# Performance work log

Measured on AMD Instinct MI355X. Metric: run time of the kernel, lower is better.

Reference implementation:

```python
import jax, jax.numpy as jnp
import numpy as np

N = 100000   # nodes
S = 2        # layout samples per graph
G = 8        # graphs in batch
E = 400000   # directed edges
MID = 256    # mid_ch
L = 4        # n_layer
CLN = 2      # concat_last_n
IN_CH = 53 + 32 + 6 * 23 + 6 * 3 + 6 * 4  # 265


def setup_inputs() -> dict:
    key = jax.random.key(0)
    ks = jax.random.split(key, 16)
    f = lambda k, sh: jax.random.normal(k, sh, dtype=jnp.float32)
    return {
        "x_feat": f(ks[0], (N, 53)),
        "dim_feat": f(ks[1], (N, 6, 23)),
        "layout_feat": f(ks[2], (N, S, 6, 4)),
        "tile_feat": f(ks[3], (G, S, 6, 3)),
        "opcode_embed": f(ks[4], (121, 32)) * 0.02,
        "preW": f(ks[5], (IN_CH, MID)) * 0.05,
        "preb": jnp.zeros((MID,), jnp.float32),
        "convWl": f(ks[6], (L, MID, MID // 2)) * 0.05,
        "convWr": f(ks[7], (L, MID, MID // 2)) * 0.05,
        "convb": jnp.zeros((L, MID // 2), jnp.float32),
        "revWl": f(ks[8], (L, MID, MID // 2)) * 0.05,
        "revWr": f(ks[9], (L, MID, MID // 2)) * 0.05,
        "revb": jnp.zeros((L, MID // 2), jnp.float32),
        "headW": f(ks[10], (MID * CLN, 1)) * 0.05,
        "headb": jnp.zeros((1,), jnp.float32),
        "node_opcode": jax.random.randint(ks[11], (N,), 0, 121),
        "batch": jnp.sort(jax.random.randint(ks[12], (N,), 0, G)),
        "edge_index": jax.random.randint(ks[13], (2, E), 0, N),
    }


def _sage(x, src, tgt, inv_deg, Wl, Wr, b):
    # PyG SAGEConv: out = lin_l(mean_{j->i} x_j) + lin_r(x_i) + bias
    # x: [S, N, C]; gather messages from src, scatter-add into tgt.
    agg = jnp.zeros_like(x).at[:, tgt].add(x[:, src])
    agg = agg * inv_deg[None, :, None]
    return (jnp.einsum('snc,co->sno', agg, Wl)
            + jnp.einsum('snc,co->sno', x, Wr) + b)


def reference(x_feat, dim_feat, layout_feat, tile_feat, opcode_embed,
              preW, preb, convWl, convWr, convb, revWl, revWr, revb,
              headW, headb, node_opcode, batch, edge_index):
    op = opcode_embed[node_opcode]                       # [N, 32]
    base = jnp.concatenate([x_feat, op, dim_feat.reshape(N, -1)], axis=-1)
    x = jnp.concatenate([
        jnp.broadcast_to(base[None], (S,) + base.shape),          # [S,N,223]
        layout_feat.transpose(1, 0, 2, 3).reshape(S, N, -1),       # [S,N,24]
        tile_feat[batch].transpose(1, 0, 2, 3).reshape(S, N, -1),  # [S,N,18]
    ], axis=-1)                                                    # [S,N,265]
    x = jax.nn.relu(x @ preW + preb)                               # [S,N,MID]

    src, tgt = edge_index[0], edge_index[1]
    one = jnp.ones((E,), x.dtype)
    inv_fwd = 1.0 / jnp.maximum(jnp.zeros((N,), x.dtype).at[tgt].add(one), 1.0)
    inv_rev = 1.0 / jnp.maximum(jnp.zeros((N,), x.dtype).at[src].add(one), 1.0)

    xs = []
    for i in range(L):
        x = jnp.concatenate([
            _sage(x, src, tgt, inv_fwd, convWl[i], convWr[i], convb[i]),
            _sage(x, tgt, src, inv_rev, revWl[i], revWr[i], revb[i]),
        ], axis=-1)
        x = jax.nn.relu(x)
        if i >= L - CLN:
            xs.append(x)
    x = jnp.concatenate(xs, axis=-1)                     # [S, N, MID*CLN]

    pooled = jnp.zeros((S, G, x.shape[-1]), x.dtype).at[:, batch].add(x)
    out = pooled @ headW + headb                         # [S, G, 1]
    return out.transpose(1, 0, 2)                        # [G, S, 1]
```

## Files before the change

### kernel.cpp

```cpp
#include <hip/hip_runtime.h>
#include <hip/hip_bf16.h>

#define N_NODES 100000
#define S_SAMP 2
#define G_GRAPH 8
#define E_EDGES 400000
#define NLAYER 4
#define IN_CH 265
#define KPRE 384
#define MT128 ((N_NODES + 127) / 128)
#define NPAD (MT128 * 128)
#define NG128 ((MT128 + 7) / 8)
#define NB1 ((N_NODES + 1023) / 1024)

typedef unsigned short u16;
typedef unsigned int u32;
typedef short bf16x8 __attribute__((ext_vector_type(8)));
typedef float f32x4 __attribute__((ext_vector_type(4)));

__device__ __forceinline__ float b2f(u16 u) {
    union { u32 i; float f; } x; x.i = ((u32)u) << 16; return x.f;
}
__device__ __forceinline__ u16 f2b(float f) {
    __hip_bfloat16 h = __float2bfloat16(f);
    return *reinterpret_cast<u16*>(&h);
}

__device__ __forceinline__ void gl_lds16(const u16* g, u16* l) {
    __builtin_amdgcn_global_load_lds(
        (const __attribute__((address_space(1))) void*)g,
        (__attribute__((address_space(3))) void*)l, 16, 0, 0);
}

__global__ __launch_bounds__(256) void build_s_k(const float* __restrict__ xf,
                                                 const float* __restrict__ dimf,
                                                 const float* __restrict__ layf,
                                                 const float* __restrict__ tilef,
                                                 const float* __restrict__ opemb,
                                                 const int* __restrict__ opcode,
                                                 const int* __restrict__ batch,
                                                 int s, u16* __restrict__ xin) {
    int item = blockIdx.x * blockDim.x + threadIdx.x;
    int n = item / 67;
    if (n >= N_NODES) return;
    int base = (item - n * 67) * 4;
    int opc = opcode[n];
    int g = batch[n];
    ushort4 o;
    u16* op = &o.x;
    #pragma unroll
    for (int u = 0; u < 4; u++) {
        int c = base + u;
        float v = 0.0f;
        if (c < 53)       v = xf[(size_t)n * 53 + c];
        else if (c < 85)  v = opemb[opc * 32 + (c - 53)];
        else if (c < 223) v = dimf[(size_t)n * 138 + (c - 85)];
        else if (c < 247) v = layf[((size_t)n * 2 + s) * 24 + (c - 223)];
        else if (c < 265) v = tilef[((size_t)g * 2 + s) * 18 + (c - 247)];
        op[u] = f2b(v);
    }
    *(ushort4*)(xin + (size_t)n * KPRE + base) = o;
}

__global__ void pack_w_k(const float* __restrict__ cWl, const float* __restrict__ rWl,
                         const float* __restrict__ cWr, const float* __restrict__ rWr,
                         const float* __restrict__ cb,  const float* __restrict__ rb,
                         u16* __restrict__ Wt, float* __restrict__ bcat) {
    int idx = blockIdx.x * blockDim.x + threadIdx.x;
    if (idx < NLAYER * 512 * 256) {
        int l = idx >> 17;
        int r = idx & 131071;
        int j = r >> 8;
        int k = r & 255;
        int jj = j & 255;
        int half = j >> 8;
        int sub = jj >> 7;
        int col = jj & 127;
        const float* src = half ? (sub ? rWl : cWl) : (sub ? rWr : cWr);
        Wt[idx] = f2b(src[((size_t)l * 256 + k) * 128 + col]);
    }
    if (idx < NLAYER * 512) {
        int l = idx >> 9;
        int j = idx & 511;
        float v = 0.0f;
        if (j < 256) v = (j < 128) ? cb[l * 128 + j] : rb[l * 128 + (j - 128)];
        bcat[idx] = v;
    }
}

__global__ void pack_pre_k(const float* __restrict__ preW, u16* __restrict__ preWt) {
    int idx = blockIdx.x * blockDim.x + threadIdx.x;
    if (idx >= 256 * KPRE) return;
    int j = idx / KPRE;
    int k = idx - j * KPRE;
    preWt[idx] = (k < IN_CH) ? f2b(preW[(size_t)k * 256 + j]) : (u16)0;
}

__global__ void deg_k(const int* __restrict__ ei, int* __restrict__ degF,
                      int* __restrict__ degR) {
    int e = blockIdx.x * blockDim.x + threadIdx.x;
    if (e < E_EDGES) {
        atomicAdd(&degF[ei[E_EDGES + e]], 1);
        atomicAdd(&degR[ei[e]], 1);
    }
}

__global__ __launch_bounds__(1024) void scan1_k(const int* __restrict__ degF,
                                                const int* __restrict__ degR,
                                                int* __restrict__ rpF,
                                                int* __restrict__ rpR,
                                                int* __restrict__ bsum) {
    const int* deg = blockIdx.y ? degR : degF;
    int* rp = blockIdx.y ? rpR : rpF;
    __shared__ int buf[1024];
    int i = blockIdx.x * 1024 + threadIdx.x;
    int v = (i < N_NODES) ? deg[i] : 0;
    buf[threadIdx.x] = v;
    __syncthreads();
    for (int off = 1; off < 1024; off <<= 1) {
        int t = (threadIdx.x >= off) ? buf[threadIdx.x - off] : 0;
        __syncthreads();
        buf[threadIdx.x] += t;
        __syncthreads();
    }
    if (i < N_NODES) rp[i] = buf[threadIdx.x] - v;
    if (threadIdx.x == 1023) bsum[blockIdx.y * NB1 + blockIdx.x] = buf[1023];
}

__global__ __launch_bounds__(256) void scan2_k(int* __restrict__ bsum,
                                               int* __restrict__ rpF,
                                               int* __restrict__ rpR) {
    __shared__ int buf[2][128];
    int half = threadIdx.x >> 7;
    int t = threadIdx.x & 127;
    int v = (t < NB1) ? bsum[half * NB1 + t] : 0;
    buf[half][t] = v;
    __syncthreads();
    for (int off = 1; off < 128; off <<= 1) {
        int x = (t >= off) ? buf[half][t - off] : 0;
        __syncthreads();
        buf[half][t] += x;
        __syncthreads();
    }
    if (t < NB1) bsum[half * NB1 + t] = buf[half][t] - v;
    if (t == NB1) (half ? rpR : rpF)[N_NODES] = buf[half][NB1 - 1];
}

__global__ void scan3_k(const int* __restrict__ bsum, int* __restrict__ rpF,
                        int* __restrict__ rpR) {
    int* rp = blockIdx.y ? rpR : rpF;
    int i = blockIdx.x * 1024 + threadIdx.x;
    if (i < N_NODES) rp[i] += bsum[blockIdx.y * NB1 + blockIdx.x];
}

__global__ void inv_cursor_k(const int* __restrict__ degF, const int* __restrict__ degR,
                             const int* __restrict__ rpF, const int* __restrict__ rpR,
                             float* __restrict__ invF, float* __restrict__ invR,
                             int* __restrict__ curF, int* __restrict__ curR) {
    int i = blockIdx.x * blockDim.x + threadIdx.x;
    if (i < N_NODES) {
        invF[i] = 1.0f / fmaxf((float)degF[i], 1.0f);
        invR[i] = 1.0f / fmaxf((float)degR[i], 1.0f);
        curF[i] = rpF[i];
        curR[i] = rpR[i];
    }
}

__global__ void fill_k(const int* __restrict__ ei, int* __restrict__ curF,
                       int* __restrict__ curR, int* __restrict__ colF,
                       int* __restrict__ colR) {
    int e = blockIdx.x * blockDim.x + threadIdx.x;
    if (e < E_EDGES) {
        int s = ei[e], t = ei[E_EDGES + e];
        colF[atomicAdd(&curF[t], 1)] = s;
        colR[atomicAdd(&curR[s], 1)] = t;
    }
}

template <bool RELU_OUT, int NCHUNK, int COLT>
__global__ __launch_bounds__(256) void mmB_k(const u16* __restrict__ A,
                                             const u16* __restrict__ Bt,
                                             const float* __restrict__ bias,
                                             u16* __restrict__ C0,
                                             u16* __restrict__ C1,
                                             int M) {
    __shared__ u16 As[128 * 128];
    __shared__ u16 Bs[64 * 128];
    constexpr int K = NCHUNK * 128;

    int bid = blockIdx.x;
    int x = bid & 7;
    int q = bid >> 3;
    int c = q % COLT;
    int g = q / COLT;
    int rowTile = g * 8 + x;
    if (rowTile >= MT128) return;
    int rowBase = rowTile * 128;
    int colBase = c * 64;

    int tid = threadIdx.x;
    int wv = tid >> 6;
    int lane = tid & 63;
    int quad = lane >> 4;
    int l16 = lane & 15;
    int rsub = lane >> 4;
    int sl = lane & 15;

    f32x4 acc[2][4] = {};

    for (int ci = 0; ci < NCHUNK; ci++) {
        int k0 = ci * 128;
        #pragma unroll
        for (int i = 0; i < 8; i++) {
            int r = wv * 32 + 4 * i + rsub;
            int ch = sl ^ (r & 15);
            gl_lds16(A + (size_t)(rowBase + r) * K + k0 + ch * 8,
                     As + (wv * 32 + 4 * i) * 128);
        }
        #pragma unroll
        for (int i = 0; i < 4; i++) {
            int r = wv * 16 + 4 * i + rsub;
            int ch = sl ^ (r & 15);
            gl_lds16(Bt + (size_t)(colBase + r) * K + k0 + ch * 8,
                     Bs + (wv * 16 + 4 * i) * 128);
        }
        __syncthreads();
        #pragma unroll
        for (int ks = 0; ks < 4; ks++) {
            int ca = ks * 4 + quad;
            bf16x8 af[2];
            #pragma unroll
            for (int rf = 0; rf < 2; rf++) {
                int ra = wv * 32 + rf * 16 + l16;
                af[rf] = *(const bf16x8*)(As + ra * 128 + (ca ^ (ra & 15)) * 8);
            }
            #pragma unroll
            for (int cf = 0; cf < 4; cf++) {
                int rb = cf * 16 + l16;
                bf16x8 bf = *(const bf16x8*)(Bs + rb * 128 + (ca ^ (rb & 15)) * 8);
                acc[0][cf] = __builtin_amdgcn_mfma_f32_16x16x32_bf16(af[0], bf, acc[0][cf], 0, 0, 0);
                acc[1][cf] = __builtin_amdgcn_mfma_f32_16x16x32_bf16(af[1], bf, acc[1][cf], 0, 0, 0);
            }
        }
        if (ci + 1 < NCHUNK) __syncthreads();
    }

    u16* dst = (colBase < 256) ? C0 : C1;
    int cb = colBase & 255;
    #pragma unroll
    for (int rf = 0; rf < 2; rf++) {
        #pragma unroll
        for (int cf = 0; cf < 4; cf++) {
            int col = cb + cf * 16 + l16;
            float bv = bias[colBase + cf * 16 + l16];
            #pragma unroll
            for (int r = 0; r < 4; r++) {
                int row = rowBase + wv * 32 + rf * 16 + quad * 4 + r;
                if (row < M) {
                    float v = acc[rf][cf][r] + bv;
                    if (RELU_OUT) v = fmaxf(v, 0.0f);
                    dst[(size_t)row * 256 + col] = f2b(v);
                }
            }
        }
    }
}

template <bool DOT>
__global__ __launch_bounds__(256) void agg_k(const int* __restrict__ rpF,
                                             const int* __restrict__ colF,
                                             const int* __restrict__ rpR,
                                             const int* __restrict__ colR,
                                             const float* __restrict__ invF,
                                             const float* __restrict__ invR,
                                             const u16* __restrict__ H,
                                             u16* __restrict__ Xn,
                                             const float* __restrict__ w,
                                             float* __restrict__ dotbuf) {
    int n = (blockIdx.x * blockDim.x + threadIdx.x) >> 6;
    if (n >= N_NODES) return;
    int lane = threadIdx.x & 63;
    int half = lane >> 5;
    int l32 = lane & 31;
    const int* rp  = half ? rpR : rpF;
    const int* col = half ? colR : colF;
    float inv = half ? invR[n] : invF[n];
    const u16* Hb = H + half * 128 + 4 * l32;

    float a0 = 0, a1 = 0, a2 = 0, a3 = 0;
    int b = rp[n], e = rp[n + 1];
    int j = b;
    for (; j + 7 < e; j += 8) {
        int c0 = col[j],     c1 = col[j + 1], c2 = col[j + 2], c3 = col[j + 3];
        int c4 = col[j + 4], c5 = col[j + 5], c6 = col[j + 6], c7 = col[j + 7];
        ushort4 h0 = *(const ushort4*)(Hb + (size_t)c0 * 256);
        ushort4 h1 = *(const ushort4*)(Hb + (size_t)c1 * 256);
        ushort4 h2 = *(const ushort4*)(Hb + (size_t)c2 * 256);
        ushort4 h3 = *(const ushort4*)(Hb + (size_t)c3 * 256);
        ushort4 h4 = *(const ushort4*)(Hb + (size_t)c4 * 256);
        ushort4 h5 = *(const ushort4*)(Hb + (size_t)c5 * 256);
        ushort4 h6 = *(const ushort4*)(Hb + (size_t)c6 * 256);
        ushort4 h7 = *(const ushort4*)(Hb + (size_t)c7 * 256);
        a0 += b2f(h0.x) + b2f(h1.x) + b2f(h2.x) + b2f(h3.x)
            + b2f(h4.x) + b2f(h5.x) + b2f(h6.x) + b2f(h7.x);
        a1 += b2f(h0.y) + b2f(h1.y) + b2f(h2.y) + b2f(h3.y)
            + b2f(h4.y) + b2f(h5.y) + b2f(h6.y) + b2f(h7.y);
        a2 += b2f(h0.z) + b2f(h1.z) + b2f(h2.z) + b2f(h3.z)
            + b2f(h4.z) + b2f(h5.z) + b2f(h6.z) + b2f(h7.z);
        a3 += b2f(h0.w) + b2f(h1.w) + b2f(h2.w) + b2f(h3.w)
            + b2f(h4.w) + b2f(h5.w) + b2f(h6.w) + b2f(h7.w);
    }
    for (; j + 3 < e; j += 4) {
        int c0 = col[j], c1 = col[j + 1], c2 = col[j + 2], c3 = col[j + 3];
        ushort4 h0 = *(const ushort4*)(Hb + (size_t)c0 * 256);
        ushort4 h1 = *(const ushort4*)(Hb + (size_t)c1 * 256);
        ushort4 h2 = *(const ushort4*)(Hb + (size_t)c2 * 256);
        ushort4 h3 = *(const ushort4*)(Hb + (size_t)c3 * 256);
        a0 += b2f(h0.x) + b2f(h1.x) + b2f(h2.x) + b2f(h3.x);
        a1 += b2f(h0.y) + b2f(h1.y) + b2f(h2.y) + b2f(h3.y);
        a2 += b2f(h0.z) + b2f(h1.z) + b2f(h2.z) + b2f(h3.z);
        a3 += b2f(h0.w) + b2f(h1.w) + b2f(h2.w) + b2f(h3.w);
    }
    for (; j < e; j++) {
        int c = col[j];
        ushort4 h = *(const ushort4*)(Hb + (size_t)c * 256);
        a0 += b2f(h.x); a1 += b2f(h.y); a2 += b2f(h.z); a3 += b2f(h.w);
    }
    u16* xp = Xn + (size_t)n * 256 + 4 * lane;
    ushort4 xv = *(const ushort4*)xp;
    float v0 = fmaxf(b2f(xv.x) + a0 * inv, 0.0f);
    float v1 = fmaxf(b2f(xv.y) + a1 * inv, 0.0f);
    float v2 = fmaxf(b2f(xv.z) + a2 * inv, 0.0f);
    float v3 = fmaxf(b2f(xv.w) + a3 * inv, 0.0f);
    ushort4 o;
    o.x = f2b(v0); o.y = f2b(v1); o.z = f2b(v2); o.w = f2b(v3);
    *(ushort4*)xp = o;
    if (DOT) {
        float4 wv4 = *(const float4*)(w + 4 * lane);
        float d = v0 * wv4.x + v1 * wv4.y + v2 * wv4.z + v3 * wv4.w;
        #pragma unroll
        for (int off = 32; off > 0; off >>= 1) d += __shfl_down(d, off);
        if (lane == 0) dotbuf[n] = d;
    }
}

__global__ void out_init_k(float* __restrict__ out, const float* __restrict__ headb) {
    int i = threadIdx.x;
    if (i < G_GRAPH * S_SAMP) out[i] = headb[0];
}

__global__ __launch_bounds__(256) void reduce_k(const float* __restrict__ dotbuf,
                                                const int* __restrict__ batch,
                                                float* __restrict__ out, int s) {
    __shared__ float part[G_GRAPH];
    if (threadIdx.x < G_GRAPH) part[threadIdx.x] = 0.0f;
    __syncthreads();
    for (int i = blockIdx.x * 256 + threadIdx.x; i < N_NODES; i += gridDim.x * 256)
        atomicAdd(&part[batch[i]], dotbuf[i]);
    __syncthreads();
    if (threadIdx.x < G_GRAPH)
        atomicAdd(&out[threadIdx.x * S_SAMP + s], part[threadIdx.x]);
}

extern "C" void kernel_launch(void* const* d_in, const int* in_sizes, int n_in,
                              void* d_out, int out_size, void* d_ws, size_t ws_size,
                              hipStream_t stream) {
    const float* x_feat      = (const float*)d_in[0];
    const float* dim_feat    = (const float*)d_in[1];
    const float* layout_feat = (const float*)d_in[2];
    const float* tile_feat   = (const float*)d_in[3];
    const float* opemb       = (const float*)d_in[4];
    const float* preW        = (const float*)d_in[5];
    const float* preb        = (const float*)d_in[6];
    const float* convWl      = (const float*)d_in[7];
    const float* convWr      = (const float*)d_in[8];
    const float* convb       = (const float*)d_in[9];
    const float* revWl       = (const float*)d_in[10];
    const float* revWr       = (const float*)d_in[11];
    const float* revb        = (const float*)d_in[12];
    const float* headW       = (const float*)d_in[13];
    const float* headb       = (const float*)d_in[14];
    const int*   node_opcode = (const int*)d_in[15];
    const int*   batch       = (const int*)d_in[16];
    const int*   edge_index  = (const int*)d_in[17];
    float* out = (float*)d_out;

    char* ws = (char*)d_ws;
    size_t off = 0;
    auto alloc = [&](size_t nbytes) {
        char* p = ws + off;
        off += (nbytes + 255) & ~(size_t)255;
        return p;
    };
    u16* XA    = (u16*)alloc((size_t)NPAD * 256 * 2);
    u16* XB    = (u16*)alloc((size_t)NPAD * 256 * 2);
    u16* XinH  = (u16*)alloc((size_t)NPAD * KPRE * 2);
    u16* Wt    = (u16*)alloc((size_t)NLAYER * 512 * 256 * 2);
    u16* preWt = (u16*)alloc((size_t)256 * KPRE * 2);
    float* bcat   = (float*)alloc(NLAYER * 512 * 4);
    float* dotbuf = (float*)alloc((size_t)N_NODES * 4);
    int* degF  = (int*)alloc(N_NODES * 4);
    int* degR  = (int*)alloc(N_NODES * 4);
    int* rpF   = (int*)alloc((N_NODES + 1) * 4);
    int* rpR   = (int*)alloc((N_NODES + 1) * 4);
    int* curF  = (int*)alloc(N_NODES * 4);
    int* curR  = (int*)alloc(N_NODES * 4);
    int* colF  = (int*)alloc(E_EDGES * 4);
    int* colR  = (int*)alloc(E_EDGES * 4);
    int* bsum  = (int*)alloc(2 * NB1 * 4);
    float* invF = (float*)alloc(N_NODES * 4);
    float* invR = (float*)alloc(N_NODES * 4);

    hipMemsetAsync(degF, 0, N_NODES * 4, stream);
    hipMemsetAsync(degR, 0, N_NODES * 4, stream);

    pack_w_k<<<(NLAYER * 512 * 256 + 255) / 256, 256, 0, stream>>>(
        convWl, revWl, convWr, revWr, convb, revb, Wt, bcat);
    pack_pre_k<<<(256 * KPRE + 255) / 256, 256, 0, stream>>>(preW, preWt);
    deg_k<<<(E_EDGES + 255) / 256, 256, 0, stream>>>(edge_index, degF, degR);
    scan1_k<<<dim3(NB1, 2), 1024, 0, stream>>>(degF, degR, rpF, rpR, bsum);
    scan2_k<<<1, 256, 0, stream>>>(bsum, rpF, rpR);
    scan3_k<<<dim3(NB1, 2), 1024, 0, stream>>>(bsum, rpF, rpR);
    inv_cursor_k<<<(N_NODES + 255) / 256, 256, 0, stream>>>(
        degF, degR, rpF, rpR, invF, invR, curF, curR);
    fill_k<<<(E_EDGES + 255) / 256, 256, 0, stream>>>(edge_index, curF, curR, colF, colR);
    out_init_k<<<1, 64, 0, stream>>>(out, headb);

    const int gridPre = NG128 * 8 * 4;
    const int gridL   = NG128 * 8 * 8;
    const int gridAgg = (N_NODES * 64 + 255) / 256;

    for (int s = 0; s < S_SAMP; s++) {
        build_s_k<<<(N_NODES * 67 + 255) / 256, 256, 0, stream>>>(
            x_feat, dim_feat, layout_feat, tile_feat, opemb, node_opcode,
            batch, s, XinH);
        mmB_k<true, 3, 4><<<gridPre, 256, 0, stream>>>(
            XinH, preWt, preb, XA, XA, N_NODES);

        u16* ins[NLAYER]  = {XA, XB, XA, XB};
        u16* outs[NLAYER] = {XB, XA, XB, XA};
        for (int l = 0; l < NLAYER; l++) {
            mmB_k<false, 2, 8><<<gridL, 256, 0, stream>>>(
                ins[l], Wt + (size_t)l * 512 * 256, bcat + (size_t)l * 512,
                outs[l], XinH, N_NODES);
            if (l < 2) {
                agg_k<false><<<gridAgg, 256, 0, stream>>>(
                    rpF, colF, rpR, colR, invF, invR, XinH, outs[l],
                    nullptr, nullptr);
            } else {
                agg_k<true><<<gridAgg, 256, 0, stream>>>(
                    rpF, colF, rpR, colR, invF, invR, XinH, outs[l],
                    headW + (l == 2 ? 0 : 256), dotbuf);
                reduce_k<<<128, 256, 0, stream>>>(dotbuf, batch, out, s);
            }
        }
    }
}
```

Before: 1.399 ms.

## Split pre-projection into shared base GEMM plus per-sample layout/tile correction

The input projection is split into two parts. The 223 sample-independent feature columns are multiplied once in a K=256 GEMM shared by both samples. The per-sample layout (24 columns) and tile (18 columns) contributions are added by a lightweight kernel that also applies ReLU, with the tile term precomputed per graph and sample. This avoids building and multiplying a 384-wide input twice, at the cost of an extra 100000x256 intermediate buffer and an FMA-heavy fix-up pass per sample. The pre-GEMM bias is added before bf16 rounding of Xmid, so the rounding point changes slightly.

```diff
diff --git a/kernel.cpp b/kernel.cpp
--- a/kernel.cpp
+++ b/kernel.cpp
@@ -7,7 +7,7 @@
 #define E_EDGES 400000
 #define NLAYER 4
 #define IN_CH 265
-#define KPRE 384
+#define KBASE 256
 #define MT128 ((N_NODES + 127) / 128)
 #define NPAD (MT128 * 128)
 #define NG128 ((MT128 + 7) / 8)
@@ -32,20 +32,16 @@
         (__attribute__((address_space(3))) void*)l, 16, 0, 0);
 }
 
-__global__ __launch_bounds__(256) void build_s_k(const float* __restrict__ xf,
-                                                 const float* __restrict__ dimf,
-                                                 const float* __restrict__ layf,
-                                                 const float* __restrict__ tilef,
-                                                 const float* __restrict__ opemb,
-                                                 const int* __restrict__ opcode,
-                                                 const int* __restrict__ batch,
-                                                 int s, u16* __restrict__ xin) {
+__global__ __launch_bounds__(256) void build_base_k(const float* __restrict__ xf,
+                                                    const float* __restrict__ dimf,
+                                                    const float* __restrict__ opemb,
+                                                    const int* __restrict__ opcode,
+                                                    u16* __restrict__ xb) {
     int item = blockIdx.x * blockDim.x + threadIdx.x;
-    int n = item / 67;
+    int n = item >> 6;
     if (n >= N_NODES) return;
-    int base = (item - n * 67) * 4;
+    int base = (item & 63) * 4;
     int opc = opcode[n];
-    int g = batch[n];
     ushort4 o;
     u16* op = &o.x;
     #pragma unroll
@@ -55,11 +51,9 @@
         if (c < 53)       v = xf[(size_t)n * 53 + c];
         else if (c < 85)  v = opemb[opc * 32 + (c - 53)];
         else if (c < 223) v = dimf[(size_t)n * 138 + (c - 85)];
-        else if (c < 247) v = layf[((size_t)n * 2 + s) * 24 + (c - 223)];
-        else if (c < 265) v = tilef[((size_t)g * 2 + s) * 18 + (c - 247)];
         op[u] = f2b(v);
     }
-    *(ushort4*)(xin + (size_t)n * KPRE + base) = o;
+    *(ushort4*)(xb + (size_t)n * KBASE + base) = o;
 }
 
 __global__ void pack_w_k(const float* __restrict__ cWl, const float* __restrict__ rWl,
@@ -90,10 +84,23 @@
 
 __global__ void pack_pre_k(const float* __restrict__ preW, u16* __restrict__ preWt) {
     int idx = blockIdx.x * blockDim.x + threadIdx.x;
-    if (idx >= 256 * KPRE) return;
-    int j = idx / KPRE;
-    int k = idx - j * KPRE;
-    preWt[idx] = (k < IN_CH) ? f2b(preW[(size_t)k * 256 + j]) : (u16)0;
+    if (idx >= 256 * KBASE) return;
+    int j = idx >> 8;
+    int k = idx & 255;
+    preWt[idx] = (k < 223) ? f2b(preW[(size_t)k * 256 + j]) : (u16)0;
+}
+
+__global__ void tvec_k(const float* __restrict__ tilef, const float* __restrict__ preW,
+                       float* __restrict__ tvec) {
+    int idx = blockIdx.x * blockDim.x + threadIdx.x;
+    if (idx >= G_GRAPH * S_SAMP * 256) return;
+    int c = idx & 255;
+    int gs = idx >> 8;
+    float a = 0.0f;
+    #pragma unroll
+    for (int k = 0; k < 18; k++)
+        a += tilef[gs * 18 + k] * preW[(size_t)(247 + k) * 256 + c];
+    tvec[idx] = a;
 }
 
 __global__ void deg_k(const int* __restrict__ ei, int* __restrict__ degF,
@@ -263,6 +270,55 @@
                 }
             }
         }
+    }
+}
+
+__global__ __launch_bounds__(256) void pre_fix_k(const u16* __restrict__ Xmid,
+                                                 const float* __restrict__ layf,
+                                                 const float* __restrict__ preW,
+                                                 const float* __restrict__ tvec,
+                                                 const int* __restrict__ batch,
+                                                 int s, u16* __restrict__ X0) {
+    __shared__ float tv[G_GRAPH * 256];
+    for (int i = threadIdx.x; i < G_GRAPH * 256; i += 256) {
+        int g = i >> 8, c = i & 255;
+        tv[i] = tvec[(g * S_SAMP + s) * 256 + c];
+    }
+    __syncthreads();
+
+    int wv = threadIdx.x >> 6;
+    int lane = threadIdx.x & 63;
+    int c0 = lane * 4;
+
+    float4 W[24];
+    #pragma unroll
+    for (int k = 0; k < 24; k++)
+        W[k] = *(const float4*)(preW + (size_t)(223 + k) * 256 + c0);
+
+    for (int n = blockIdx.x * 4 + wv; n < N_NODES; n += gridDim.x * 4) {
+        int g = batch[n];
+        float4 L4[6];
+        const float4* lp = (const float4*)(layf + ((size_t)n * S_SAMP + s) * 24);
+        #pragma unroll
+        for (int q = 0; q < 6; q++) L4[q] = lp[q];
+        const float* l = (const float*)L4;
+        float4 t4 = *(const float4*)&tv[g * 256 + c0];
+        float a0 = t4.x, a1 = t4.y, a2 = t4.z, a3 = t4.w;
+        #pragma unroll
+        for (int k = 0; k < 24; k++) {
+            float lk = l[k];
+            a0 += lk * W[k].x;
+            a1 += lk * W[k].y;
+            a2 += lk * W[k].z;
+            a3 += lk * W[k].w;
+        }
+        ushort4 m = *(const ushort4*)(Xmid + (size_t)n * 256 + c0);
+        ushort4 o;
+        o.x = f2b(fmaxf(b2f(m.x) + a0, 0.0f));
+        o.y = f2b(fmaxf(b2f(m.y) + a1, 0.0f));
+        o.z = f2b(fmaxf(b2f(m.z) + a2, 0.0f));
+        o.w = f2b(fmaxf(b2f(m.w) + a3, 0.0f));
+        *(ushort4*)(X0 + (size_t)n * 256 + c0) = o;
     }
 }
 
@@ -394,10 +450,12 @@
     };
     u16* XA    = (u16*)alloc((size_t)NPAD * 256 * 2);
     u16* XB    = (u16*)alloc((size_t)NPAD * 256 * 2);
-    u16* XinH  = (u16*)alloc((size_t)NPAD * KPRE * 2);
+    u16* XbH   = (u16*)alloc((size_t)NPAD * 256 * 2);
+    u16* Xmid  = (u16*)alloc((size_t)NPAD * 256 * 2);
     u16* Wt    = (u16*)alloc((size_t)NLAYER * 512 * 256 * 2);
-    u16* preWt = (u16*)alloc((size_t)256 * KPRE * 2);
+    u16* preWt = (u16*)alloc((size_t)256 * KBASE * 2);
     float* bcat   = (float*)alloc(NLAYER * 512 * 4);
+    float* tvec   = (float*)alloc(G_GRAPH * S_SAMP * 256 * 4);
     float* dotbuf = (float*)alloc((size_t)N_NODES * 4);
     int* degF  = (int*)alloc(N_NODES * 4);
     int* degR  = (int*)alloc(N_NODES * 4);
@@ -416,7 +474,9 @@
 
     pack_w_k<<<(NLAYER * 512 * 256 + 255) / 256, 256, 0, stream>>>(
         convWl, revWl, convWr, revWr, convb, revb, Wt, bcat);
-    pack_pre_k<<<(256 * KPRE + 255) / 256, 256, 0, stream>>>(preW, preWt);
+    pack_pre_k<<<(256 * KBASE + 255) / 256, 256, 0, stream>>>(preW, preWt);
+    tvec_k<<<(G_GRAPH * S_SAMP * 256 + 255) / 256, 256, 0, stream>>>(
+        tile_feat, preW, tvec);
     deg_k<<<(E_EDGES + 255) / 256, 256, 0, stream>>>(edge_index, degF, degR);
     scan1_k<<<dim3(NB1, 2), 1024, 0, stream>>>(degF, degR, rpF, rpR, bsum);
     scan2_k<<<1, 256, 0, stream>>>(bsum, rpF, rpR);
@@ -426,30 +486,31 @@
     fill_k<<<(E_EDGES + 255) / 256, 256, 0, stream>>>(edge_index, curF, curR, colF, colR);
     out_init_k<<<1, 64, 0, stream>>>(out, headb);
 
-    const int gridPre = NG128 * 8 * 4;
+    build_base_k<<<(N_NODES * 64 + 255) / 256, 256, 0, stream>>>(
+        x_feat, dim_feat, opemb, node_opcode, XbH);
+    mmB_k<false, 2, 4><<<NG128 * 8 * 4, 256, 0, stream>>>(
+        XbH, preWt, preb, Xmid, Xmid, N_NODES);
+
     const int gridL   = NG128 * 8 * 8;
     const int gridAgg = (N_NODES * 64 + 255) / 256;
 
     for (int s = 0; s < S_SAMP; s++) {
-        build_s_k<<<(N_NODES * 67 + 255) / 256, 256, 0, stream>>>(
-            x_feat, dim_feat, layout_feat, tile_feat, opemb, node_opcode,
-            batch, s, XinH);
-        mmB_k<true, 3, 4><<<gridPre, 256, 0, stream>>>(
-            XinH, preWt, preb, XA, XA, N_NODES);
+        pre_fix_k<<<2048, 256, 0, stream>>>(
+            Xmid, layout_feat, preW, tvec, batch, s, XA);
 
         u16* ins[NLAYER]  = {XA, XB, XA, XB};
         u16* outs[NLAYER] = {XB, XA, XB, XA};
         for (int l = 0; l < NLAYER; l++) {
             mmB_k<false, 2, 8><<<gridL, 256, 0, stream>>>(
                 ins[l], Wt + (size_t)l * 512 * 256, bcat + (size_t)l * 512,
-                outs[l], XinH, N_NODES);
+                outs[l], XbH, N_NODES);
             if (l < 2) {
                 agg_k<false><<<gridAgg, 256, 0, stream>>>(
-                    rpF, colF, rpR, colR, invF, invR, XinH, outs[l],
+                    rpF, colF, rpR, colR, invF, invR, XbH, outs[l],
                     nullptr, nullptr);
             } else {
                 agg_k<true><<<gridAgg, 256, 0, stream>>>(
-                    rpF, colF, rpR, colR, invF, invR, XinH, outs[l],
+                    rpF, colF, rpR, colR, invF, invR, XbH, outs[l],
                     headW + (l == 2 ? 0 : 256), dotbuf);
                 reduce_k<<<128, 256, 0, stream>>>(dotbuf, batch, out, s);
             }
```

After: 1.365 ms. 2.5% less time.
